# Performance work log

Hardware: AMD Instinct MI355X
Metric: run time of the kernel (lower is better)

Reference implementation:

```python
import math
import jax, jax.numpy as jnp
import numpy as np

NUM_BINS = 8
TRANS = 8
LEFT, RIGHT = -1.0, 1.0
MIN_W = MIN_H = MIN_D = 1.0e-4


def setup_inputs() -> dict:
    key = jax.random.key(0)
    ks = jax.random.split(key, 8)
    B, D, H, OUT = 524288, 16, 256, TRANS * (3 * NUM_BINS - 1)
    x = jax.random.uniform(ks[0], (B, D), jnp.float32, -0.99, 0.99)
    W0 = jax.random.normal(ks[1], (8, H), jnp.float32) * (1.0 / math.sqrt(8))
    b0 = jnp.zeros((H,), jnp.float32)
    W1 = jax.random.normal(ks[2], (H, H), jnp.float32) * (1.0 / math.sqrt(H))
    b1 = jnp.zeros((H,), jnp.float32)
    Wout = jax.random.normal(ks[3], (H, OUT), jnp.float32) * (0.1 / math.sqrt(H))
    bout = jnp.zeros((OUT,), jnp.float32)
    return {"x": x, "W0": W0, "b0": b0, "W1": W1, "b1": b1, "Wout": Wout, "bout": bout}


def _rq_spline(x, raw_w, raw_h, raw_d):
    # x: [B, T]; raw_w/raw_h: [B, T, K]; raw_d: [B, T, K-1]
    span = RIGHT - LEFT
    const = math.log(math.exp(1.0 - MIN_D) - 1.0)
    widths = jax.nn.softmax(raw_w, axis=-1)
    heights = jax.nn.softmax(raw_h, axis=-1)
    derivs = jax.nn.softplus(raw_d + const) + MIN_D
    widths = span * (MIN_W + (1.0 - MIN_W * NUM_BINS) * widths)
    heights = span * (MIN_H + (1.0 - MIN_H * NUM_BINS) * heights)
    edge_x = LEFT + jnp.pad(jnp.cumsum(widths, axis=-1), ((0, 0), (0, 0), (1, 0)))
    edge_y = LEFT + jnp.pad(jnp.cumsum(heights, axis=-1), ((0, 0), (0, 0), (1, 0)))
    derivs = jnp.pad(derivs, ((0, 0), (0, 0), (1, 1)), constant_values=1.0)
    out_mask = (x <= LEFT + 1e-3) | (x >= RIGHT - 1e-3)
    x_in = jnp.where(out_mask, 0.0, x)
    # searchsorted(right=True) - 1 == count of edges <= x_in, minus 1
    idx = jnp.clip(jnp.sum(edge_x <= x_in[..., None], axis=-1) - 1, 0, NUM_BINS - 1)
    g = lambda a: jnp.take_along_axis(a, idx[..., None], axis=-1)[..., 0]
    xk, yk = g(edge_x), g(edge_y)
    wk, hk = g(widths), g(heights)
    dk, dk1 = g(derivs), g(derivs[..., 1:])
    sk = hk / wk
    eps = (x_in - xk) / wk
    eps_term = eps * (1.0 - eps)
    eps2 = eps * eps
    beta = sk + (dk1 + dk - 2.0 * sk) * eps_term
    alpha = hk * (sk * eps2 + dk * eps_term)
    output = jnp.where(out_mask, x, yk + alpha / beta)
    logdet = (2.0 * jnp.log(sk)
              + jnp.log(dk1 * eps2 + 2.0 * sk * eps_term + dk * (1.0 - eps) ** 2)
              - 2.0 * jnp.log(beta))
    logdet = jnp.where(out_mask, 0.0, logdet)
    return output, logdet


def reference(x, W0, b0, W1, b1, Wout, bout):
    x1 = x[..., :TRANS]   # transformed half (mask == True)
    x2 = x[..., TRANS:]   # conditioning half
    h = jax.nn.relu(x2 @ W0 + b0)
    h = jax.nn.relu(h @ W1 + b1)
    raw = (h @ Wout + bout).reshape(x.shape[0], TRANS, 3 * NUM_BINS - 1)
    raw_w = raw[..., :NUM_BINS]
    raw_h = raw[..., NUM_BINS:2 * NUM_BINS]
    raw_d = raw[..., 2 * NUM_BINS:]
    y1, logdet = _rq_spline(x1, raw_w, raw_h, raw_d)
    out = jnp.concatenate([y1, x2], axis=-1)
    return out, jnp.sum(logdet, axis=-1)
```

## Files before the change

### kernel.cpp

```cpp
#include <hip/hip_runtime.h>
#include <hip/hip_bf16.h>


typedef __bf16 bf16x8 __attribute__((ext_vector_type(8)));
typedef __bf16 bf16x4v __attribute__((ext_vector_type(4)));
typedef float  f32x8 __attribute__((ext_vector_type(8)));
typedef float  f32x4 __attribute__((ext_vector_type(4)));
typedef float  f32x2 __attribute__((ext_vector_type(2)));

#define MFMA16(a,b,c) __builtin_amdgcn_mfma_f32_16x16x32_bf16((a),(b),(c),0,0,0)

#define SW_W1_OFF 8192
#define SW_WO_OFF 73728
#define SW_TOTAL  122880

#define ROWS    128
#define HSTRIDE 264
#define LOG2E   1.44269504f
#define LN2     0.69314718f
#define SPCONST 0.7806568f
#define ZSENT  (-0.00015680f)

__global__ void prep_kernel(const float* __restrict__ W0,
                            const float* __restrict__ W1,
                            const float* __restrict__ Wout,
                            const float* __restrict__ bout,
                            __bf16* __restrict__ sw)
{
  int i = blockIdx.x * 256 + threadIdx.x;
  if (i >= SW_TOTAL + 192) return;
  if (i >= SW_TOTAL){
    int np = i - SW_TOTAL;
    int t = np / 24, p = np % 24;
    float* boutp = (float*)(sw + SW_TOTAL);
    boutp[np] = (p < 23) ? bout[t*23 + p] * LOG2E : 0.f;
    return;
  }
  const float* src; int K, N, NT, li;
  bool wo = false;
  if (i < SW_W1_OFF)      { src = W0;   K = 8;   N = 256; NT = 16; li = i; }
  else if (i < SW_WO_OFF) { src = W1;   K = 256; N = 256; NT = 16; li = i - SW_W1_OFF; }
  else { src = Wout; K = 256; N = 184; NT = 12; li = i - SW_WO_OFF; wo = true; }
  int j    = li & 7;
  int l    = (li >> 3) & 63;
  int rest = li >> 9;
  int nt   = rest % NT;
  int kb   = rest / NT;
  int k = kb * 32 + ((l >> 4) << 3) + j;
  int n = nt * 16 + (l & 15);
  float v;
  if (wo){
    int t = n / 24, p = n % 24;
    v = (p < 23 && k < K) ? Wout[k*184 + t*23 + p] * LOG2E : 0.f;
  } else {
    v = (k < K && n < N) ? src[k * N + n] : 0.f;
  }
  sw[i] = (__bf16)v;
}

__device__ __forceinline__ bf16x4v relu_cvt4(f32x4 acc, float4 bb){
  f32x4 s;
  s[0] = acc[0] + bb.x; s[1] = acc[1] + bb.y;
  s[2] = acc[2] + bb.z; s[3] = acc[3] + bb.w;
  f32x4 z = {0.f, 0.f, 0.f, 0.f};
  s = __builtin_elementwise_max(s, z);
  return __builtin_convertvector(s, bf16x4v);
}

__device__ __forceinline__ bf16x4v add_cvt4(f32x4 acc, float4 bb){
  f32x4 s;
  s[0] = acc[0] + bb.x; s[1] = acc[1] + bb.y;
  s[2] = acc[2] + bb.z; s[3] = acc[3] + bb.w;
  return __builtin_convertvector(s, bf16x4v);
}

__global__ __launch_bounds__(512, 4)
void fused_kernel(const float* __restrict__ x,
                  const float* __restrict__ b0v,
                  const float* __restrict__ b1v,
                  const __bf16* __restrict__ sw,
                  float* __restrict__ out,
                  int nrows)
{
  __shared__ __align__(16) unsigned char smem[ROWS * HSTRIDE * 2];
  __bf16* hbuf = (__bf16*)smem;
  __bf16* rawb = hbuf;

  const int tid  = threadIdx.x;
  const int wave = tid >> 6;
  const int lane = tid & 63;
  const int quad = lane >> 4;
  const int l16  = lane & 15;
  const int row0 = blockIdx.x * ROWS;

  const __bf16* swW1 = sw + SW_W1_OFF;
  const __bf16* swWo = sw + SW_WO_OFF;
  const float* boutp = (const float*)(sw + SW_TOTAL);
  const f32x4 z4 = {0.f, 0.f, 0.f, 0.f};

  if (tid < 2*ROWS){
    int r = tid >> 1, hf = tid & 1;
    long g = (long)row0 + r;
    *(float4*)(out + g*16 + 8 + hf*4) = *(const float4*)(x + g*16 + 8 + hf*4);
  }

  const int mq = wave >> 1;
  const int nh = wave & 1;

  {
    bf16x8 bfr[4];
    #pragma unroll
    for (int nt = 0; nt < 4; nt++){
      bf16x8 b = {};
      if (quad == 0){
        const float* xp = x + (long)(row0 + (nh*4 + nt)*16 + l16)*16 + 8;
        float4 u = *(const float4*)xp;
        float4 v = *(const float4*)(xp + 4);
        f32x8 xf; xf[0]=u.x; xf[1]=u.y; xf[2]=u.z; xf[3]=u.w;
                  xf[4]=v.x; xf[5]=v.y; xf[6]=v.z; xf[7]=v.w;
        b = __builtin_convertvector(xf, bf16x8);
      }
      bfr[nt] = b;
    }
    #pragma unroll
    for (int mi = 0; mi < 4; mi++){
      int mt = mq*4 + mi;
      bf16x8 a = *(const bf16x8*)(sw + (mt*64 + lane)*8);
      float4 bb = *(const float4*)(b0v + mt*16 + quad*4);
      #pragma unroll
      for (int nt = 0; nt < 4; nt++){
        f32x4 acc = MFMA16(a, bfr[nt], z4);
        *(bf16x4v*)(hbuf + ((nh*4+nt)*16 + l16)*HSTRIDE + mt*16 + quad*4) = relu_cvt4(acc, bb);
      }
    }
  }
  __syncthreads();

  {
    f32x4 acc[4][4];
    #pragma unroll
    for (int mi=0;mi<4;mi++)
      #pragma unroll
      for (int bt=0;bt<4;bt++) acc[mi][bt] = z4;
    #pragma unroll
    for (int kb=0;kb<8;kb++){
      bf16x8 hf[4];
      #pragma unroll
      for (int bt=0;bt<4;bt++)
        hf[bt] = *(const bf16x8*)(hbuf + ((nh*4+bt)*16 + l16)*HSTRIDE + kb*32 + quad*8);
      #pragma unroll
      for (int mi=0;mi<4;mi++){
        bf16x8 a = *(const bf16x8*)(swW1 + ((kb*16 + mq*4 + mi)*64 + lane)*8);
        #pragma unroll
        for (int bt=0;bt<4;bt++)
          acc[mi][bt] = MFMA16(a, hf[bt], acc[mi][bt]);
      }
    }
    __syncthreads();
    #pragma unroll
    for (int mi=0;mi<4;mi++){
      int mt = mq*4 + mi;
      float4 bb = *(const float4*)(b1v + mt*16 + quad*4);
      #pragma unroll
      for (int bt=0;bt<4;bt++)
        *(bf16x4v*)(hbuf + ((nh*4+bt)*16 + l16)*HSTRIDE + mt*16 + quad*4) = relu_cvt4(acc[mi][bt], bb);
    }
  }
  __syncthreads();

  {
    const int nc = wave & 3;
    const int mh = wave >> 2;
    f32x4 acc[4][3];
    #pragma unroll
    for (int bt=0;bt<4;bt++)
      #pragma unroll
      for (int mi=0;mi<3;mi++) acc[bt][mi] = z4;
    #pragma unroll
    for (int kb=0;kb<8;kb++){
      bf16x8 hf[4];
      #pragma unroll
      for (int bt=0;bt<4;bt++)
        hf[bt] = *(const bf16x8*)(hbuf + ((mh*4+bt)*16 + l16)*HSTRIDE + kb*32 + quad*8);
      #pragma unroll
      for (int mi=0;mi<3;mi++){
        bf16x8 a = *(const bf16x8*)(swWo + ((kb*12 + nc*3 + mi)*64 + lane)*8);
        #pragma unroll
        for (int bt=0;bt<4;bt++)
          acc[bt][mi] = MFMA16(a, hf[bt], acc[bt][mi]);
      }
    }
    __syncthreads();
    #pragma unroll
    for (int mi=0;mi<3;mi++){
      int mt = nc*3 + mi;
      float4 bb = *(const float4*)(boutp + mt*16 + quad*4);
      #pragma unroll
      for (int bt=0;bt<4;bt++){
        int row = (mh*4+bt)*16 + l16;
        *(bf16x4v*)(rawb + row*HSTRIDE + mt*16 + quad*4) = add_cvt4(acc[bt][mi], bb);
      }
    }
  }
  __syncthreads();

  float ldv[2];
  #pragma unroll
  for (int pp = 0; pp < 2; pp++){
    int p   = tid + pp*512;
    int row = p >> 3;
    int t   = p & 7;
    long gr = row0 + row;
    float xv = x[gr*16 + t];

    const __bf16* rr = rawb + row*HSTRIDE + t*24;
    bf16x8 v0 = *(const bf16x8*)(rr);
    bf16x8 v1 = *(const bf16x8*)(rr + 8);
    bf16x8 v2 = *(const bf16x8*)(rr + 16);

    f32x2 ewh[8];
    f32x2 sum = {0.f, 0.f};
    #pragma unroll
    for (int i=0;i<8;i++){
      f32x2 e;
      e[0] = __builtin_amdgcn_exp2f((float)v0[i]);
      e[1] = __builtin_amdgcn_exp2f((float)v1[i]);
      ewh[i] = e; sum += e;
    }
    f32x2 scale;
    scale[0] = 1.9984f * __builtin_amdgcn_rcpf(sum[0]);
    scale[1] = 1.9984f * __builtin_amdgcn_rcpf(sum[1]);
    const f32x2 off2 = {2e-4f, 2e-4f};

    bool msk = (xv <= -0.999f) || (xv >= 0.999f);
    float xin = msk ? 0.f : xv;

    f32x2 whi = ewh[0]*scale + off2;
    f32x2 ec; ec[0] = -1.f + whi[0]; ec[1] = -1.f + whi[1];
    f32x2 xyk = {-1.f, -1.f};
    f32x2 whk = whi;
    float zk = ZSENT, zk1 = (float)v2[0];
    #pragma unroll
    for (int i=1;i<8;i++){
      whi = ewh[i]*scale + off2;
      bool le = (ec[0] <= xin);
      xyk = le ? ec : xyk;
      whk = le ? whi : whk;
      zk  = le ? (float)v2[i-1] : zk;
      zk1 = le ? ((i==7) ? ZSENT : (float)v2[i]) : zk1;
      ec += whi;
    }

    float za = zk + SPCONST, zb = zk1 + SPCONST;
    float dk  = (fmaxf(za,0.f) + __builtin_amdgcn_logf(1.f + __builtin_amdgcn_exp2f(-fabsf(za))))*LN2 + 1e-4f;
    float dk1 = (fmaxf(zb,0.f) + __builtin_amdgcn_logf(1.f + __builtin_amdgcn_exp2f(-fabsf(zb))))*LN2 + 1e-4f;

    float rwk = __builtin_amdgcn_rcpf(whk[0]);
    float sk  = whk[1] * rwk;
    float eps = (xin - xyk[0]) * rwk;
    float om  = 1.f - eps;
    float et  = eps * om;
    float e2  = eps * eps;
    float beta  = sk + (dk1 + dk - 2.f*sk) * et;
    float rb    = __builtin_amdgcn_rcpf(beta);
    float alpha = whk[1] * (sk*e2 + dk*et);
    float yv  = msk ? xv : (xyk[1] + alpha * rb);
    float num = dk1*e2 + 2.f*sk*et + dk*om*om;
    float ld  = msk ? 0.f : __builtin_amdgcn_logf(sk*sk*num*rb*rb) * LN2;

    out[gr*16 + t] = yv;
    ldv[pp] = ld;
  }

  float s0 = ldv[0], s1 = ldv[1];
  #pragma unroll
  for (int m = 1; m < 8; m <<= 1){
    s0 += __shfl_xor(s0, m);
    s1 += __shfl_xor(s1, m);
  }
  if ((lane & 7) == 0){
    int r = tid >> 3;
    out[(long)nrows*16 + row0 + r]      = s0;
    out[(long)nrows*16 + row0 + r + 64] = s1;
  }
}

extern "C" void kernel_launch(void* const* d_in, const int* in_sizes, int n_in,
                              void* d_out, int out_size, void* d_ws, size_t ws_size,
                              hipStream_t stream)
{
  const float* x    = (const float*)d_in[0];
  const float* W0   = (const float*)d_in[1];
  const float* b0   = (const float*)d_in[2];
  const float* W1   = (const float*)d_in[3];
  const float* b1   = (const float*)d_in[4];
  const float* Wout = (const float*)d_in[5];
  const float* bout = (const float*)d_in[6];
  float* out = (float*)d_out;
  __bf16* sw = (__bf16*)d_ws;

  int nrows = in_sizes[0] / 16;
  int ntiles = nrows / ROWS;

  prep_kernel<<<(SW_TOTAL + 192 + 255)/256, 256, 0, stream>>>(W0, W1, Wout, bout, sw);
  fused_kernel<<<ntiles, 512, 0, stream>>>(x, b0, b1, sw, out, nrows);
}
```

Measured before the change: 219.3 us.

## Warp-specialize fused kernel: MLP waves and spline waves pipelined across tiles

Blocks grow to 1024 threads. Eight waves run the three MLP GEMMs on tile i while the other eight run the rational-quadratic spline epilogue on tile i-1. Separate LDS buffers for hidden activations and raw outputs let the two stages overlap, and each block loops over 8 tiles. This aims to hide the transcendental-heavy epilogue behind MFMA work, at the cost of twice the LDS per block, fewer resident blocks, and a one-tile pipeline fill and drain.

```diff
diff --git a/kernel.cpp b/kernel.cpp
--- a/kernel.cpp
+++ b/kernel.cpp
@@ -15,6 +15,7 @@
 #define SW_TOTAL  122880
 
 #define ROWS    128
+#define IT      8
 #define HSTRIDE 264
 #define LOG2E   1.44269504f
 #define LN2     0.69314718f
@@ -74,7 +75,7 @@
   return __builtin_convertvector(s, bf16x4v);
 }
 
-__global__ __launch_bounds__(512, 4)
+__global__ __launch_bounds__(1024, 4)
 void fused_kernel(const float* __restrict__ x,
                   const float* __restrict__ b0v,
                   const float* __restrict__ b1v,
@@ -82,206 +83,237 @@
                   float* __restrict__ out,
                   int nrows)
 {
-  __shared__ __align__(16) unsigned char smem[ROWS * HSTRIDE * 2];
-  __bf16* hbuf = (__bf16*)smem;
-  __bf16* rawb = hbuf;
+  __shared__ __align__(16) unsigned char smemA[ROWS * HSTRIDE * 2];
+  __shared__ __align__(16) unsigned char smemB[ROWS * HSTRIDE * 2];
+  __bf16* hbuf = (__bf16*)smemA;
+  __bf16* rawb = (__bf16*)smemB;
 
   const int tid  = threadIdx.x;
   const int wave = tid >> 6;
+  const bool isW = wave < 8;
   const int lane = tid & 63;
   const int quad = lane >> 4;
   const int l16  = lane & 15;
-  const int row0 = blockIdx.x * ROWS;
+  const int tid2 = tid - 512;
 
   const __bf16* swW1 = sw + SW_W1_OFF;
   const __bf16* swWo = sw + SW_WO_OFF;
   const float* boutp = (const float*)(sw + SW_TOTAL);
   const f32x4 z4 = {0.f, 0.f, 0.f, 0.f};
 
-  if (tid < 2*ROWS){
-    int r = tid >> 1, hf = tid & 1;
-    long g = (long)row0 + r;
-    *(float4*)(out + g*16 + 8 + hf*4) = *(const float4*)(x + g*16 + 8 + hf*4);
-  }
-
   const int mq = wave >> 1;
   const int nh = wave & 1;
 
-  {
-    bf16x8 bfr[4];
-    #pragma unroll
-    for (int nt = 0; nt < 4; nt++){
-      bf16x8 b = {};
-      if (quad == 0){
-        const float* xp = x + (long)(row0 + (nh*4 + nt)*16 + l16)*16 + 8;
-        float4 u = *(const float4*)xp;
-        float4 v = *(const float4*)(xp + 4);
-        f32x8 xf; xf[0]=u.x; xf[1]=u.y; xf[2]=u.z; xf[3]=u.w;
-                  xf[4]=v.x; xf[5]=v.y; xf[6]=v.z; xf[7]=v.w;
-        b = __builtin_convertvector(xf, bf16x8);
-      }
-      bfr[nt] = b;
-    }
-    #pragma unroll
-    for (int mi = 0; mi < 4; mi++){
-      int mt = mq*4 + mi;
-      bf16x8 a = *(const bf16x8*)(sw + (mt*64 + lane)*8);
-      float4 bb = *(const float4*)(b0v + mt*16 + quad*4);
+  for (int it = 0; it <= IT; ++it){
+    const int row0W = (blockIdx.x * IT + it) * ROWS;
+    const int row0E = (blockIdx.x * IT + it - 1) * ROWS;
+    const bool doW = isW && (it < IT);
+    const bool doE = (!isW) && (it > 0);
+
+    bf16x8 ev0[2], ev1[2], ev2[2];
+    f32x2 xyk_s[2], whk_s[2];
+    float zk_s[2], zk1_s[2], xv_s[2];
+    bool  msk_s[2];
+    f32x4 acc2[4][4];
+
+    if (doW){
+      bf16x8 bfr[4];
       #pragma unroll
       for (int nt = 0; nt < 4; nt++){
-        f32x4 acc = MFMA16(a, bfr[nt], z4);
-        *(bf16x4v*)(hbuf + ((nh*4+nt)*16 + l16)*HSTRIDE + mt*16 + quad*4) = relu_cvt4(acc, bb);
-      }
-    }
-  }
-  __syncthreads();
-
-  {
-    f32x4 acc[4][4];
-    #pragma unroll
-    for (int mi=0;mi<4;mi++)
-      #pragma unroll
-      for (int bt=0;bt<4;bt++) acc[mi][bt] = z4;
-    #pragma unroll
-    for (int kb=0;kb<8;kb++){
-      bf16x8 hf[4];
-      #pragma unroll
-      for (int bt=0;bt<4;bt++)
-        hf[bt] = *(const bf16x8*)(hbuf + ((nh*4+bt)*16 + l16)*HSTRIDE + kb*32 + quad*8);
-      #pragma unroll
-      for (int mi=0;mi<4;mi++){
-        bf16x8 a = *(const bf16x8*)(swW1 + ((kb*16 + mq*4 + mi)*64 + lane)*8);
-        #pragma unroll
-        for (int bt=0;bt<4;bt++)
-          acc[mi][bt] = MFMA16(a, hf[bt], acc[mi][bt]);
+        bf16x8 b = {};
+        if (quad == 0){
+          const float* xp = x + (long)(row0W + (nh*4 + nt)*16 + l16)*16 + 8;
+          float4 u = *(const float4*)xp;
+          float4 v = *(const float4*)(xp + 4);
+          f32x8 xf; xf[0]=u.x; xf[1]=u.y; xf[2]=u.z; xf[3]=u.w;
+                    xf[4]=v.x; xf[5]=v.y; xf[6]=v.z; xf[7]=v.w;
+          b = __builtin_convertvector(xf, bf16x8);
+        }
+        bfr[nt] = b;
+      }
+      #pragma unroll
+      for (int mi = 0; mi < 4; mi++){
+        int mt = mq*4 + mi;
+        bf16x8 a = *(const bf16x8*)(sw + (mt*64 + lane)*8);
+        float4 bb = *(const float4*)(b0v + mt*16 + quad*4);
+        #pragma unroll
+        for (int nt = 0; nt < 4; nt++){
+          f32x4 acc = MFMA16(a, bfr[nt], z4);
+          *(bf16x4v*)(hbuf + ((nh*4+nt)*16 + l16)*HSTRIDE + mt*16 + quad*4) = relu_cvt4(acc, bb);
+        }
+      }
+    } else if (doE){
+      if (tid2 < 2*ROWS){
+        int r = tid2 >> 1, hf = tid2 & 1;
+        long g = (long)row0E + r;
+        *(float4*)(out + g*16 + 8 + hf*4) = *(const float4*)(x + g*16 + 8 + hf*4);
+      }
+      #pragma unroll
+      for (int pp = 0; pp < 2; pp++){
+        int p   = tid2 + pp*512;
+        int row = p >> 3;
+        int t   = p & 7;
+        const __bf16* rr = rawb + row*HSTRIDE + t*24;
+        ev0[pp] = *(const bf16x8*)(rr);
+        ev1[pp] = *(const bf16x8*)(rr + 8);
+        ev2[pp] = *(const bf16x8*)(rr + 16);
+        xv_s[pp] = x[((long)row0E + row)*16 + t];
       }
     }
     __syncthreads();
-    #pragma unroll
-    for (int mi=0;mi<4;mi++){
-      int mt = mq*4 + mi;
-      float4 bb = *(const float4*)(b1v + mt*16 + quad*4);
-      #pragma unroll
-      for (int bt=0;bt<4;bt++)
-        *(bf16x4v*)(hbuf + ((nh*4+bt)*16 + l16)*HSTRIDE + mt*16 + quad*4) = relu_cvt4(acc[mi][bt], bb);
-    }
-  }
-  __syncthreads();
-
-  {
-    const int nc = wave & 3;
-    const int mh = wave >> 2;
-    f32x4 acc[4][3];
-    #pragma unroll
-    for (int bt=0;bt<4;bt++)
-      #pragma unroll
-      for (int mi=0;mi<3;mi++) acc[bt][mi] = z4;
-    #pragma unroll
-    for (int kb=0;kb<8;kb++){
-      bf16x8 hf[4];
-      #pragma unroll
-      for (int bt=0;bt<4;bt++)
-        hf[bt] = *(const bf16x8*)(hbuf + ((mh*4+bt)*16 + l16)*HSTRIDE + kb*32 + quad*8);
-      #pragma unroll
-      for (int mi=0;mi<3;mi++){
-        bf16x8 a = *(const bf16x8*)(swWo + ((kb*12 + nc*3 + mi)*64 + lane)*8);
+
+    if (doW){
+      #pragma unroll
+      for (int mi=0;mi<4;mi++)
+        #pragma unroll
+        for (int bt=0;bt<4;bt++) acc2[mi][bt] = z4;
+      #pragma unroll
+      for (int kb=0;kb<8;kb++){
+        bf16x8 hf[4];
         #pragma unroll
         for (int bt=0;bt<4;bt++)
-          acc[bt][mi] = MFMA16(a, hf[bt], acc[bt][mi]);
+          hf[bt] = *(const bf16x8*)(hbuf + ((nh*4+bt)*16 + l16)*HSTRIDE + kb*32 + quad*8);
+        #pragma unroll
+        for (int mi=0;mi<4;mi++){
+          bf16x8 a = *(const bf16x8*)(swW1 + ((kb*16 + mq*4 + mi)*64 + lane)*8);
+          #pragma unroll
+          for (int bt=0;bt<4;bt++)
+            acc2[mi][bt] = MFMA16(a, hf[bt], acc2[mi][bt]);
+        }
+      }
+    } else if (doE){
+      #pragma unroll
+      for (int pp = 0; pp < 2; pp++){
+        f32x2 ewh[8];
+        f32x2 sum = {0.f, 0.f};
+        #pragma unroll
+        for (int i=0;i<8;i++){
+          f32x2 e;
+          e[0] = __builtin_amdgcn_exp2f((float)ev0[pp][i]);
+          e[1] = __builtin_amdgcn_exp2f((float)ev1[pp][i]);
+          ewh[i] = e; sum += e;
+        }
+        f32x2 scale;
+        scale[0] = 1.9984f * __builtin_amdgcn_rcpf(sum[0]);
+        scale[1] = 1.9984f * __builtin_amdgcn_rcpf(sum[1]);
+        const f32x2 off2 = {2e-4f, 2e-4f};
+
+        float xv = xv_s[pp];
+        bool msk = (xv <= -0.999f) || (xv >= 0.999f);
+        float xin = msk ? 0.f : xv;
+
+        f32x2 whi = ewh[0]*scale + off2;
+        f32x2 ec; ec[0] = -1.f + whi[0]; ec[1] = -1.f + whi[1];
+        f32x2 xyk = {-1.f, -1.f};
+        f32x2 whk = whi;
+        float zk = ZSENT, zk1 = (float)ev2[pp][0];
+        #pragma unroll
+        for (int i=1;i<8;i++){
+          whi = ewh[i]*scale + off2;
+          bool le = (ec[0] <= xin);
+          xyk = le ? ec : xyk;
+          whk = le ? whi : whk;
+          zk  = le ? (float)ev2[pp][i-1] : zk;
+          zk1 = le ? ((i==7) ? ZSENT : (float)ev2[pp][i]) : zk1;
+          ec += whi;
+        }
+        xyk_s[pp] = xyk; whk_s[pp] = whk;
+        zk_s[pp] = zk; zk1_s[pp] = zk1; msk_s[pp] = msk;
       }
     }
     __syncthreads();
-    #pragma unroll
-    for (int mi=0;mi<3;mi++){
-      int mt = nc*3 + mi;
-      float4 bb = *(const float4*)(boutp + mt*16 + quad*4);
-      #pragma unroll
-      for (int bt=0;bt<4;bt++){
-        int row = (mh*4+bt)*16 + l16;
-        *(bf16x4v*)(rawb + row*HSTRIDE + mt*16 + quad*4) = add_cvt4(acc[bt][mi], bb);
+
+    if (doW){
+      #pragma unroll
+      for (int mi=0;mi<4;mi++){
+        int mt = mq*4 + mi;
+        float4 bb = *(const float4*)(b1v + mt*16 + quad*4);
+        #pragma unroll
+        for (int bt=0;bt<4;bt++)
+          *(bf16x4v*)(hbuf + ((nh*4+bt)*16 + l16)*HSTRIDE + mt*16 + quad*4) =
+              relu_cvt4(acc2[mi][bt], bb);
       }
     }
-  }
-  __syncthreads();
-
-  float ldv[2];
-  #pragma unroll
-  for (int pp = 0; pp < 2; pp++){
-    int p   = tid + pp*512;
-    int row = p >> 3;
-    int t   = p & 7;
-    long gr = row0 + row;
-    float xv = x[gr*16 + t];
-
-    const __bf16* rr = rawb + row*HSTRIDE + t*24;
-    bf16x8 v0 = *(const bf16x8*)(rr);
-    bf16x8 v1 = *(const bf16x8*)(rr + 8);
-    bf16x8 v2 = *(const bf16x8*)(rr + 16);
-
-    f32x2 ewh[8];
-    f32x2 sum = {0.f, 0.f};
-    #pragma unroll
-    for (int i=0;i<8;i++){
-      f32x2 e;
-      e[0] = __builtin_amdgcn_exp2f((float)v0[i]);
-      e[1] = __builtin_amdgcn_exp2f((float)v1[i]);
-      ewh[i] = e; sum += e;
+    __syncthreads();
+
+    if (doW){
+      const int nc = wave & 3;
+      const int mh = wave >> 2;
+      f32x4 acc[4][3];
+      #pragma unroll
+      for (int bt=0;bt<4;bt++)
+        #pragma unroll
+        for (int mi=0;mi<3;mi++) acc[bt][mi] = z4;
+      #pragma unroll
+      for (int kb=0;kb<8;kb++){
+        bf16x8 hf[4];
+        #pragma unroll
+        for (int bt=0;bt<4;bt++)
+          hf[bt] = *(const bf16x8*)(hbuf + ((mh*4+bt)*16 + l16)*HSTRIDE + kb*32 + quad*8);
+        #pragma unroll
+        for (int mi=0;mi<3;mi++){
+          bf16x8 a = *(const bf16x8*)(swWo + ((kb*12 + nc*3 + mi)*64 + lane)*8);
+          #pragma unroll
+          for (int bt=0;bt<4;bt++)
+            acc[bt][mi] = MFMA16(a, hf[bt], acc[bt][mi]);
+        }
+      }
+      #pragma unroll
+      for (int mi=0;mi<3;mi++){
+        int mt = nc*3 + mi;
+        float4 bb = *(const float4*)(boutp + mt*16 + quad*4);
+        #pragma unroll
+        for (int bt=0;bt<4;bt++){
+          int row = (mh*4+bt)*16 + l16;
+          *(bf16x4v*)(rawb + row*HSTRIDE + mt*16 + quad*4) = add_cvt4(acc[bt][mi], bb);
+        }
+      }
+    } else if (doE){
+      float ldv[2];
+      #pragma unroll
+      for (int pp = 0; pp < 2; pp++){
+        int p   = tid2 + pp*512;
+        int row = p >> 3;
+        int t   = p & 7;
+        long gr = row0E + row;
+        float xv = xv_s[pp];
+        bool msk = msk_s[pp];
+        float xin = msk ? 0.f : xv;
+        f32x2 xyk = xyk_s[pp], whk = whk_s[pp];
+
+        float za = zk_s[pp] + SPCONST, zb = zk1_s[pp] + SPCONST;
+        float dk  = (fmaxf(za,0.f) + __builtin_amdgcn_logf(1.f + __builtin_amdgcn_exp2f(-fabsf(za))))*LN2 + 1e-4f;
+        float dk1 = (fmaxf(zb,0.f) + __builtin_amdgcn_logf(1.f + __builtin_amdgcn_exp2f(-fabsf(zb))))*LN2 + 1e-4f;
+
+        float rwk = __builtin_amdgcn_rcpf(whk[0]);
+        float sk  = whk[1] * rwk;
+        float eps = (xin - xyk[0]) * rwk;
+        float om  = 1.f - eps;
+        float et  = eps * om;
+        float e2  = eps * eps;
+        float beta  = sk + (dk1 + dk - 2.f*sk) * et;
+        float rb    = __builtin_amdgcn_rcpf(beta);
+        float alpha = whk[1] * (sk*e2 + dk*et);
+        float yv  = msk ? xv : (xyk[1] + alpha * rb);
+        float num = dk1*e2 + 2.f*sk*et + dk*om*om;
+        float ld  = msk ? 0.f : __builtin_amdgcn_logf(sk*sk*num*rb*rb) * LN2;
+
+        out[gr*16 + t] = yv;
+        ldv[pp] = ld;
+      }
+      float s0 = ldv[0], s1 = ldv[1];
+      #pragma unroll
+      for (int m = 1; m < 8; m <<= 1){
+        s0 += __shfl_xor(s0, m);
+        s1 += __shfl_xor(s1, m);
+      }
+      if ((lane & 7) == 0){
+        int r = tid2 >> 3;
+        out[(long)nrows*16 + row0E + r]      = s0;
+        out[(long)nrows*16 + row0E + r + 64] = s1;
+      }
     }
-    f32x2 scale;
-    scale[0] = 1.9984f * __builtin_amdgcn_rcpf(sum[0]);
-    scale[1] = 1.9984f * __builtin_amdgcn_rcpf(sum[1]);
-    const f32x2 off2 = {2e-4f, 2e-4f};
-
-    bool msk = (xv <= -0.999f) || (xv >= 0.999f);
-    float xin = msk ? 0.f : xv;
-
-    f32x2 whi = ewh[0]*scale + off2;
-    f32x2 ec; ec[0] = -1.f + whi[0]; ec[1] = -1.f + whi[1];
-    f32x2 xyk = {-1.f, -1.f};
-    f32x2 whk = whi;
-    float zk = ZSENT, zk1 = (float)v2[0];
-    #pragma unroll
-    for (int i=1;i<8;i++){
-      whi = ewh[i]*scale + off2;
-      bool le = (ec[0] <= xin);
-      xyk = le ? ec : xyk;
-      whk = le ? whi : whk;
-      zk  = le ? (float)v2[i-1] : zk;
-      zk1 = le ? ((i==7) ? ZSENT : (float)v2[i]) : zk1;
-      ec += whi;
-    }
-
-    float za = zk + SPCONST, zb = zk1 + SPCONST;
-    float dk  = (fmaxf(za,0.f) + __builtin_amdgcn_logf(1.f + __builtin_amdgcn_exp2f(-fabsf(za))))*LN2 + 1e-4f;
-    float dk1 = (fmaxf(zb,0.f) + __builtin_amdgcn_logf(1.f + __builtin_amdgcn_exp2f(-fabsf(zb))))*LN2 + 1e-4f;
-
-    float rwk = __builtin_amdgcn_rcpf(whk[0]);
-    float sk  = whk[1] * rwk;
-    float eps = (xin - xyk[0]) * rwk;
-    float om  = 1.f - eps;
-    float et  = eps * om;
-    float e2  = eps * eps;
-    float beta  = sk + (dk1 + dk - 2.f*sk) * et;
-    float rb    = __builtin_amdgcn_rcpf(beta);
-    float alpha = whk[1] * (sk*e2 + dk*et);
-    float yv  = msk ? xv : (xyk[1] + alpha * rb);
-    float num = dk1*e2 + 2.f*sk*et + dk*om*om;
-    float ld  = msk ? 0.f : __builtin_amdgcn_logf(sk*sk*num*rb*rb) * LN2;
-
-    out[gr*16 + t] = yv;
-    ldv[pp] = ld;
-  }
-
-  float s0 = ldv[0], s1 = ldv[1];
-  #pragma unroll
-  for (int m = 1; m < 8; m <<= 1){
-    s0 += __shfl_xor(s0, m);
-    s1 += __shfl_xor(s1, m);
-  }
-  if ((lane & 7) == 0){
-    int r = tid >> 3;
-    out[(long)nrows*16 + row0 + r]      = s0;
-    out[(long)nrows*16 + row0 + r + 64] = s1;
+    __syncthreads();
   }
 }
 
@@ -299,9 +331,10 @@
   float* out = (float*)d_out;
   __bf16* sw = (__bf16*)d_ws;
 
-  int nrows = in_sizes[0] / 16;
+  int nrows  = in_sizes[0] / 16;
   int ntiles = nrows / ROWS;
+  int nblk   = ntiles / IT;
 
   prep_kernel<<<(SW_TOTAL + 192 + 255)/256, 256, 0, stream>>>(W0, W1, Wout, bout, sw);
-  fused_kernel<<<ntiles, 512, 0, stream>>>(x, b0, b1, sw, out, nrows);
-}
+  fused_kernel<<<nblk, 1024, 0, stream>>>(x, b0, b1, sw, out, nrows);
+}
```

Result: slower. 783.7 us (+257.3%).
